# Kernel tuning notes

Measured on AMD Instinct MI355X. Metric: run time of the kernel, lower is better.

Reference implementation:

```python
import jax, jax.numpy as jnp
import numpy as np
from jax import lax

FILTER_SIZE = 11
SIGMA = 1.5
K1, K2 = 0.01, 0.03
WEIGHTS = jnp.array([0.0448, 0.2856, 0.3001, 0.2363, 0.1333], dtype=jnp.float32)


def _gauss_1d(size, sigma):
    coords = jnp.arange(size, dtype=jnp.float32) - (size - 1) / 2.0
    return jax.nn.softmax(-coords ** 2 / (2.0 * sigma ** 2))


def _gaussian_filter(x, k1d):
    # separable depthwise blur, VALID padding: horizontal then vertical
    C = x.shape[1]
    size = k1d.shape[0]
    kw = jnp.broadcast_to(k1d.reshape(1, 1, 1, size), (C, 1, 1, size))  # OIHW
    kh = jnp.broadcast_to(k1d.reshape(1, 1, size, 1), (C, 1, size, 1))
    dn = ('NCHW', 'OIHW', 'NCHW')
    x = lax.conv_general_dilated(x, kw, (1, 1), 'VALID', dimension_numbers=dn, feature_group_count=C)
    x = lax.conv_general_dilated(x, kh, (1, 1), 'VALID', dimension_numbers=dn, feature_group_count=C)
    return x


def _ssim(x, y, k1d, max_val):
    c1 = (K1 * max_val) ** 2
    c2 = (K2 * max_val) ** 2
    mu1 = _gaussian_filter(x, k1d)
    mu2 = _gaussian_filter(y, k1d)
    mu1_sq, mu2_sq, mu1_mu2 = mu1 ** 2, mu2 ** 2, mu1 * mu2
    sigma1_sq = _gaussian_filter(x * x, k1d) - mu1_sq
    sigma2_sq = _gaussian_filter(y * y, k1d) - mu2_sq
    sigma12 = _gaussian_filter(x * y, k1d) - mu1_mu2
    cs_map = (2 * sigma12 + c2) / (sigma1_sq + sigma2_sq + c2)
    ssim_map = (2 * mu1_mu2 + c1) / (mu1_sq + mu2_sq + c1) * cs_map
    return ssim_map.mean(axis=(-1, -2, -3)), cs_map.mean(axis=(-1, -2, -3))


def _avg_pool2(x):
    # torch avg_pool2d(kernel=2, padding=(H%2, W%2)), count_include_pad=True
    ph, pw = x.shape[-2] % 2, x.shape[-1] % 2
    if ph or pw:
        x = jnp.pad(x, ((0, 0), (0, 0), (ph, ph), (pw, pw)))
    N, C, H, W = x.shape
    return x.reshape(N, C, H // 2, 2, W // 2, 2).mean(axis=(-3, -1))


def setup_inputs() -> dict:
    key = jax.random.key(0)
    k1, k2 = jax.random.split(key)
    shape = (32, 3, 512, 512)
    return {
        'input': jax.random.uniform(k1, shape, dtype=jnp.float32),
        'target': jax.random.uniform(k2, shape, dtype=jnp.float32),
    }


def reference(input, target):
    k1d = _gauss_1d(FILTER_SIZE, SIGMA)
    max_val = target.max() - target.min()  # module default: max_val=None
    levels = WEIGHTS.shape[0]
    x, y = input, target
    mcs = []
    ssim_val = None
    for _ in range(levels):
        ssim_val, cs = _ssim(x, y, k1d, max_val)
        mcs.append(cs)
        x = _avg_pool2(x)
        y = _avg_pool2(y)
    mcs = jnp.stack(mcs, axis=0)  # (levels, N)
    # faithful to original: ssim_val ** w[-1] broadcast inside the product
    ms = jnp.prod(mcs[:-1] ** WEIGHTS[:-1, None] * ssim_val ** WEIGHTS[-1], axis=0)
    return ms.mean()
```

## Files before the change

kernel.cpp:

```cpp
#include <hip/hip_runtime.h>
#include <cmath>

#define FILT 11

typedef float v2f __attribute__((ext_vector_type(2)));

struct GW { float w[FILT]; };

__device__ __forceinline__ unsigned enc_f(float f) {
    unsigned u = __float_as_uint(f);
    return (u & 0x80000000u) ? ~u : (u | 0x80000000u);
}
__device__ __forceinline__ float dec_f(unsigned u) {
    return (u & 0x80000000u) ? __uint_as_float(u & 0x7FFFFFFFu)
                             : __uint_as_float(~u);
}

__global__ void init_acc(unsigned* ws) {
    int t = threadIdx.x;
    if (t == 0) { ws[0] = 0u; ws[1] = 0xFFFFFFFFu; }
    for (int i = 2 + t; i < 512; i += blockDim.x) ws[i] = 0u;
}

__global__ void minmax_kernel(const float4* __restrict__ t, long n4, unsigned* mm) {
    unsigned mx = 0u, mn = 0xFFFFFFFFu;
    long stride = (long)gridDim.x * blockDim.x;
    for (long i = (long)blockIdx.x * blockDim.x + threadIdx.x; i < n4; i += stride) {
        float4 v = t[i];
        unsigned a = enc_f(v.x), b = enc_f(v.y), c = enc_f(v.z), d = enc_f(v.w);
        mx = max(mx, max(max(a, b), max(c, d)));
        mn = min(mn, min(min(a, b), min(c, d)));
    }
    for (int off = 32; off; off >>= 1) {
        mx = max(mx, (unsigned)__shfl_down((int)mx, off));
        mn = min(mn, (unsigned)__shfl_down((int)mn, off));
    }
    __shared__ unsigned smx[4], smn[4];
    int wid = threadIdx.x >> 6, lane = threadIdx.x & 63;
    if (lane == 0) { smx[wid] = mx; smn[wid] = mn; }
    __syncthreads();
    if (threadIdx.x == 0) {
        for (int i = 1; i < 4; i++) { mx = max(mx, smx[i]); mn = min(mn, smn[i]); }
        atomicMax(&mm[0], mx);
        atomicMin(&mm[1], mn);
    }
}

__global__ __launch_bounds__(256) void ssim_stream(
    const float* __restrict__ x, const float* __restrict__ y,
    int H, int W, int NC, int nstrips, int nb, int B,
    const unsigned* __restrict__ mm,
    float* __restrict__ cs_sum, float* __restrict__ ssim_sum, GW gw,
    float* __restrict__ poolx, float* __restrict__ pooly, int do_pool)
{
    __shared__ v2f ring[4][2][80];

    const int wv = threadIdx.x >> 6;
    const int lane = threadIdx.x & 63;
    const int wid = blockIdx.x * 4 + wv;
    const int total = NC * nstrips * nb;
    if (wid >= total) return;

    const int band = wid % nb;
    const int t1 = wid / nb;
    const int strip = t1 % nstrips;
    const int img = t1 / nstrips;
    const int n = img / 3;

    const int Ho = H - (FILT - 1);
    const int Wo = W - (FILT - 1);
    const int a = band * B;
    if (a >= Ho) return;
    const int out_hi = min(a + B, Ho);
    const int bEnd = out_hi + (FILT - 1);

    const int base = strip * 64;
    const float* xp = x + (size_t)img * H * W;
    const float* yp = y + (size_t)img * H * W;
    const int c0 = min(base + lane, W - 1);
    const int c1 = min(base + 64 + min(lane, 9), W - 1);
    const bool colv = (base + lane) < Wo;

    const float mv = dec_f(mm[0]) - dec_f(mm[1]);
    const float c1c = (0.01f * mv) * (0.01f * mv);
    const float c2c = (0.03f * mv) * (0.03f * mv);

    const int Wp = W >> 1;
    const size_t pbase = (size_t)img * (H >> 1) * Wp;

    v2f* bufE = &ring[wv][0][0];
    v2f* bufO = &ring[wv][1][0];

    v2f acc01[FILT], acc23[FILT];
    float acc4[FILT];
#pragma unroll
    for (int s = 0; s < FILT; s++) {
        acc01[s] = (v2f){0.f, 0.f};
        acc23[s] = (v2f){0.f, 0.f};
        acc4[s] = 0.f;
    }

    float lcs = 0.f, lss = 0.f;

    float ex0, ey0, ex1, ey1, ox0, oy0, ox1, oy1;
    {
        const float* xe = xp + (size_t)a * W;
        const float* ye = yp + (size_t)a * W;
        ex0 = xe[c0]; ey0 = ye[c0]; ex1 = xe[c1]; ey1 = ye[c1];
        ox0 = xe[W + c0]; oy0 = ye[W + c0];
        ox1 = xe[W + c1]; oy1 = ye[W + c1];
    }

#pragma unroll 1
    for (int r0 = a; r0 < bEnd; r0 += 22) {
#pragma unroll
        for (int p = 0; p < FILT; p++) {
            const int r = r0 + 2 * p;
            if (r < bEnd) {
                const bool hasO = (r + 1 < bEnd);
                const int pe = (2 * p) % FILT;
                const int po = (2 * p + 1) % FILT;

                bufE[lane] = (v2f){ex0, ey0};
                if (lane < 10) bufE[64 + lane] = (v2f){ex1, ey1};
                if (hasO) {
                    bufO[lane] = (v2f){ox0, oy0};
                    if (lane < 10) bufO[64 + lane] = (v2f){ox1, oy1};
                }

                {
                    const int re = min(r + 2, bEnd - 1);
                    const int ro = min(r + 3, bEnd - 1);
                    const float* xe = xp + (size_t)re * W;
                    const float* ye = yp + (size_t)re * W;
                    const float* xo = xp + (size_t)ro * W;
                    const float* yo = yp + (size_t)ro * W;
                    ex0 = xe[c0]; ey0 = ye[c0]; ex1 = xe[c1]; ey1 = ye[c1];
                    ox0 = xo[c0]; oy0 = yo[c0]; ox1 = xo[c1]; oy1 = yo[c1];
                }

                if (do_pool && hasO && lane < 32) {
                    const int pc = (base >> 1) + lane;
                    if (pc < Wp) {
                        float4 qe = *(const float4*)&bufE[2 * lane];
                        float4 qo = *(const float4*)&bufO[2 * lane];
                        size_t o = pbase + (size_t)(r >> 1) * Wp + pc;
                        poolx[o] = 0.25f * (qe.x + qe.z + qo.x + qo.z);
                        pooly[o] = 0.25f * (qe.y + qe.w + qo.y + qo.w);
                    }
                }

                v2f h01e = (v2f){0.f, 0.f}, h23e = (v2f){0.f, 0.f};
                float h4e = 0.f;
#pragma unroll
                for (int k = 0; k < FILT; k++) {
                    v2f v = bufE[lane + k];
                    float w = gw.w[k];
                    v2f w2 = {w, w};
                    h01e = __builtin_elementwise_fma(w2, v, h01e);
                    v2f sq = v * v;
                    h23e = __builtin_elementwise_fma(w2, sq, h23e);
                    h4e = __builtin_fmaf(w, v.x * v.y, h4e);
                }

#pragma unroll
                for (int k = 0; k < FILT; k++) {
                    const int s = (pe - k + FILT) % FILT;
                    float w = gw.w[k];
                    v2f w2 = {w, w};
                    acc01[s] = __builtin_elementwise_fma(w2, h01e, acc01[s]);
                    acc23[s] = __builtin_elementwise_fma(w2, h23e, acc23[s]);
                    acc4[s] = __builtin_fmaf(w, h4e, acc4[s]);
                }

                const int eE = (pe + 1) % FILT;
                if (r >= a + (FILT - 1) && colv) {
                    float m1 = acc01[eE].x, m2 = acc01[eE].y;
                    float mu11 = m1 * m1, mu22 = m2 * m2, mu12 = m1 * m2;
                    float s1 = acc23[eE].x - mu11;
                    float s2 = acc23[eE].y - mu22;
                    float s12 = acc4[eE] - mu12;
                    float A = 2.f * s12 + c2c, Bv = s1 + s2 + c2c;
                    float Cv = 2.f * mu12 + c1c, Dv = mu11 + mu22 + c1c;
                    float r_ = __builtin_amdgcn_rcpf(Bv * Dv);
                    lcs += A * Dv * r_;
                    lss += Cv * A * r_;
                }
                acc01[eE] = (v2f){0.f, 0.f};
                acc23[eE] = (v2f){0.f, 0.f};
                acc4[eE] = 0.f;

                if (hasO) {
                    v2f h01o = (v2f){0.f, 0.f}, h23o = (v2f){0.f, 0.f};
                    float h4o = 0.f;
#pragma unroll
                    for (int k = 0; k < FILT; k++) {
                        v2f v = bufO[lane + k];
                        float w = gw.w[k];
                        v2f w2 = {w, w};
                        h01o = __builtin_elementwise_fma(w2, v, h01o);
                        v2f sq = v * v;
                        h23o = __builtin_elementwise_fma(w2, sq, h23o);
                        h4o = __builtin_fmaf(w, v.x * v.y, h4o);
                    }
#pragma unroll
                    for (int k = 0; k < FILT; k++) {
                        const int s = (po - k + FILT) % FILT;
                        float w = gw.w[k];
                        v2f w2 = {w, w};
                        acc01[s] = __builtin_elementwise_fma(w2, h01o, acc01[s]);
                        acc23[s] = __builtin_elementwise_fma(w2, h23o, acc23[s]);
                        acc4[s] = __builtin_fmaf(w, h4o, acc4[s]);
                    }
                    const int eO = (po + 1) % FILT;
                    if (r >= a + (FILT - 1) && colv) {
                        float m1 = acc01[eO].x, m2 = acc01[eO].y;
                        float mu11 = m1 * m1, mu22 = m2 * m2, mu12 = m1 * m2;
                        float s1 = acc23[eO].x - mu11;
                        float s2 = acc23[eO].y - mu22;
                        float s12 = acc4[eO] - mu12;
                        float A = 2.f * s12 + c2c, Bv = s1 + s2 + c2c;
                        float Cv = 2.f * mu12 + c1c, Dv = mu11 + mu22 + c1c;
                        float r_ = __builtin_amdgcn_rcpf(Bv * Dv);
                        lcs += A * Dv * r_;
                        lss += Cv * A * r_;
                    }
                    acc01[eO] = (v2f){0.f, 0.f};
                    acc23[eO] = (v2f){0.f, 0.f};
                    acc4[eO] = 0.f;
                }
            }
        }
    }

    for (int off = 32; off; off >>= 1) {
        lcs += __shfl_down(lcs, off);
        lss += __shfl_down(lss, off);
    }
    if (lane == 0) {
        atomicAdd(&cs_sum[n], lcs);
        atomicAdd(&ssim_sum[n], lss);
    }
}

__global__ void final_kernel(const float* __restrict__ cs_sum,
                             const float* __restrict__ ssim_sum,
                             float* __restrict__ out)
{
    const float cnt[5] = {3.f * 502 * 502, 3.f * 246 * 246, 3.f * 118 * 118,
                          3.f * 54 * 54, 3.f * 22 * 22};
    const float wts[5] = {0.0448f, 0.2856f, 0.3001f, 0.2363f, 0.1333f};
    int n = threadIdx.x;
    float ms = 0.f;
    if (n < 32) {
        float ssim = ssim_sum[4 * 32 + n] / cnt[4];
        float t = powf(ssim, wts[4]);
        ms = 1.f;
        for (int l = 0; l < 4; l++) {
            float cs = cs_sum[l * 32 + n] / cnt[l];
            ms *= powf(cs, wts[l]) * t;
        }
    }
    for (int off = 32; off; off >>= 1) ms += __shfl_down(ms, off);
    if (threadIdx.x == 0) out[0] = ms / 32.f;
}

extern "C" void kernel_launch(void* const* d_in, const int* in_sizes, int n_in,
                              void* d_out, int out_size, void* d_ws, size_t ws_size,
                              hipStream_t stream) {
    const float* x0 = (const float*)d_in[0];
    const float* y0 = (const float*)d_in[1];
    float* out = (float*)d_out;
    float* ws = (float*)d_ws;
    unsigned* mm = (unsigned*)d_ws;
    float* cs_sum = ws + 2;
    float* ssim_sum = ws + 2 + 5 * 32;

    const int N = 32, C = 3, NC = N * C;
    const int Hs[5] = {512, 256, 128, 64, 32};
    const int Bs[5] = {64, 42, 12, 10, 8};

    float* wp = ws + 512;
    float* pxw[5] = {nullptr, nullptr, nullptr, nullptr, nullptr};
    float* pyw[5] = {nullptr, nullptr, nullptr, nullptr, nullptr};
    for (int l = 1; l < 5; l++) {
        size_t sz = (size_t)NC * Hs[l] * Hs[l];
        pxw[l] = wp; wp += sz;
        pyw[l] = wp; wp += sz;
    }
    const float* px[5] = {x0, pxw[1], pxw[2], pxw[3], pxw[4]};
    const float* py[5] = {y0, pyw[1], pyw[2], pyw[3], pyw[4]};

    GW gw;
    {
        double tmp[FILT], s = 0.0;
        for (int k = 0; k < FILT; k++) {
            double c = (double)k - (FILT - 1) / 2.0;
            tmp[k] = exp(-c * c / (2.0 * 1.5 * 1.5));
            s += tmp[k];
        }
        for (int k = 0; k < FILT; k++) gw.w[k] = (float)(tmp[k] / s);
    }

    init_acc<<<1, 256, 0, stream>>>(mm);
    long n4 = (long)NC * 512 * 512 / 4;
    minmax_kernel<<<2048, 256, 0, stream>>>((const float4*)y0, n4, mm);

    for (int l = 0; l < 5; l++) {
        int H = Hs[l];
        int Ho = H - (FILT - 1);
        int nstrips = (Ho + 63) / 64;
        int B = Bs[l];
        int nb = (Ho + B - 1) / B;
        int total_waves = NC * nstrips * nb;
        int grid = (total_waves + 3) / 4;
        int do_pool = (l < 4) ? 1 : 0;
        ssim_stream<<<grid, 256, 0, stream>>>(
            px[l], py[l], H, H, NC, nstrips, nb, B, mm,
            cs_sum + l * 32, ssim_sum + l * 32, gw,
            do_pool ? pxw[l + 1] : nullptr,
            do_pool ? pyw[l + 1] : nullptr, do_pool);
    }
    final_kernel<<<1, 64, 0, stream>>>(cs_sum, ssim_sum, out);
}
```

Before: 329.0 us.

## Fuse SSIM levels 2-4 into one per-image kernel using shared-memory pyramids

Pyramid levels 2, 3 and 4 are merged into a single kernel with one 1024-thread block per image. Level 2 streams from global memory and writes its 2x2 pooled output into shared memory, then levels 3 and 4 are computed entirely from shared memory. This removes two kernel launches and the global round trips for the small levels, which were dominated by launch and latency costs. Level 0 now runs with 1024-thread blocks instead of 256. The trade-off is heavy shared-memory use per block and only 96 blocks for the fused tail, so parallelism there is low.

```diff
diff --git a/kernel.cpp b/kernel.cpp
--- a/kernel.cpp
+++ b/kernel.cpp
@@ -46,18 +46,19 @@
     }
 }
 
-__global__ __launch_bounds__(256) void ssim_stream(
+__global__ __launch_bounds__(1024) void ssim_stream(
     const float* __restrict__ x, const float* __restrict__ y,
     int H, int W, int NC, int nstrips, int nb, int B,
     const unsigned* __restrict__ mm,
     float* __restrict__ cs_sum, float* __restrict__ ssim_sum, GW gw,
     float* __restrict__ poolx, float* __restrict__ pooly, int do_pool)
 {
-    __shared__ v2f ring[4][2][80];
+    __shared__ v2f ring[16][2][80];
 
     const int wv = threadIdx.x >> 6;
     const int lane = threadIdx.x & 63;
-    const int wid = blockIdx.x * 4 + wv;
+    const int wpb = blockDim.x >> 6;
+    const int wid = blockIdx.x * wpb + wv;
     const int total = NC * nstrips * nb;
     if (wid >= total) return;
 
@@ -162,7 +163,6 @@
                     h23e = __builtin_elementwise_fma(w2, sq, h23e);
                     h4e = __builtin_fmaf(w, v.x * v.y, h4e);
                 }
-
 #pragma unroll
                 for (int k = 0; k < FILT; k++) {
                     const int s = (pe - k + FILT) % FILT;
@@ -172,7 +172,6 @@
                     acc23[s] = __builtin_elementwise_fma(w2, h23e, acc23[s]);
                     acc4[s] = __builtin_fmaf(w, h4e, acc4[s]);
                 }
-
                 const int eE = (pe + 1) % FILT;
                 if (r >= a + (FILT - 1) && colv) {
                     float m1 = acc01[eE].x, m2 = acc01[eE].y;
@@ -240,6 +239,244 @@
     if (lane == 0) {
         atomicAdd(&cs_sum[n], lcs);
         atomicAdd(&ssim_sum[n], lss);
+    }
+}
+
+__device__ __forceinline__ void ssim_lds_strip(
+    const v2f* tile, int Wt, int Wo, int a, int out_hi, int lane,
+    float c1c, float c2c, const GW& gw, float& lcs, float& lss)
+{
+    const int bEnd = out_hi + (FILT - 1);
+    const int tl = min(lane, Wo - 1);
+    const bool colv = lane < Wo;
+
+    v2f acc01[FILT], acc23[FILT];
+    float acc4[FILT];
+#pragma unroll
+    for (int s = 0; s < FILT; s++) {
+        acc01[s] = (v2f){0.f, 0.f};
+        acc23[s] = (v2f){0.f, 0.f};
+        acc4[s] = 0.f;
+    }
+
+#pragma unroll 1
+    for (int r0 = a; r0 < bEnd; r0 += FILT) {
+#pragma unroll
+        for (int p = 0; p < FILT; p++) {
+            const int r = r0 + p;
+            if (r < bEnd) {
+                const v2f* row = tile + (size_t)r * Wt;
+                v2f h01 = (v2f){0.f, 0.f}, h23 = (v2f){0.f, 0.f};
+                float h4 = 0.f;
+#pragma unroll
+                for (int k = 0; k < FILT; k++) {
+                    v2f v = row[tl + k];
+                    float w = gw.w[k];
+                    v2f w2 = {w, w};
+                    h01 = __builtin_elementwise_fma(w2, v, h01);
+                    v2f sq = v * v;
+                    h23 = __builtin_elementwise_fma(w2, sq, h23);
+                    h4 = __builtin_fmaf(w, v.x * v.y, h4);
+                }
+#pragma unroll
+                for (int k = 0; k < FILT; k++) {
+                    const int s = (p - k + FILT) % FILT;
+                    float w = gw.w[k];
+                    v2f w2 = {w, w};
+                    acc01[s] = __builtin_elementwise_fma(w2, h01, acc01[s]);
+                    acc23[s] = __builtin_elementwise_fma(w2, h23, acc23[s]);
+                    acc4[s] = __builtin_fmaf(w, h4, acc4[s]);
+                }
+                const int e = (p + 1) % FILT;
+                if (r >= a + (FILT - 1) && colv) {
+                    float m1 = acc01[e].x, m2 = acc01[e].y;
+                    float mu11 = m1 * m1, mu22 = m2 * m2, mu12 = m1 * m2;
+                    float s1 = acc23[e].x - mu11;
+                    float s2 = acc23[e].y - mu22;
+                    float s12 = acc4[e] - mu12;
+                    float A = 2.f * s12 + c2c, Bv = s1 + s2 + c2c;
+                    float Cv = 2.f * mu12 + c1c, Dv = mu11 + mu22 + c1c;
+                    float r_ = __builtin_amdgcn_rcpf(Bv * Dv);
+                    lcs += A * Dv * r_;
+                    lss += Cv * A * r_;
+                }
+                acc01[e] = (v2f){0.f, 0.f};
+                acc23[e] = (v2f){0.f, 0.f};
+                acc4[e] = 0.f;
+            }
+        }
+    }
+}
+
+__global__ __launch_bounds__(1024) void ssim_tail(
+    const float* __restrict__ x2, const float* __restrict__ y2,
+    const unsigned* __restrict__ mm, float* __restrict__ ws2, GW gw)
+{
+    __shared__ v2f ring[16][2][80];
+    __shared__ v2f buf3[64 * 64];
+    __shared__ v2f buf4[32 * 32];
+
+    const int img = blockIdx.x;
+    const int n = img / 3;
+    const int wv = threadIdx.x >> 6;
+    const int lane = threadIdx.x & 63;
+
+    float* cs2 = ws2 + 2 + 2 * 32;
+    float* cs3 = ws2 + 2 + 3 * 32;
+    float* cs4 = ws2 + 2 + 4 * 32;
+    float* ss2 = ws2 + 2 + 5 * 32 + 2 * 32;
+    float* ss3 = ws2 + 2 + 5 * 32 + 3 * 32;
+    float* ss4 = ws2 + 2 + 5 * 32 + 4 * 32;
+
+    const float mv = dec_f(mm[0]) - dec_f(mm[1]);
+    const float c1c = (0.01f * mv) * (0.01f * mv);
+    const float c2c = (0.03f * mv) * (0.03f * mv);
+
+    {
+        const int strip = wv >> 3;
+        const int band = wv & 7;
+        const int H = 128, W = 128, Ho = 118, B = 16;
+        const int a = band * B;
+        const int out_hi = min(a + B, Ho);
+        const int bEnd = out_hi + (FILT - 1);
+        const int base = strip * 64;
+        const float* xp = x2 + (size_t)img * H * W;
+        const float* yp = y2 + (size_t)img * H * W;
+        const int c0 = min(base + lane, W - 1);
+        const int c1 = min(base + 64 + min(lane, 9), W - 1);
+        const bool colv = (base + lane) < Ho;
+
+        v2f* bufA = &ring[wv][0][0];
+        v2f* bufB = &ring[wv][1][0];
+
+        v2f acc01[FILT], acc23[FILT];
+        float acc4[FILT];
+#pragma unroll
+        for (int s = 0; s < FILT; s++) {
+            acc01[s] = (v2f){0.f, 0.f};
+            acc23[s] = (v2f){0.f, 0.f};
+            acc4[s] = 0.f;
+        }
+        float lcs = 0.f, lss = 0.f;
+
+        const float* xr = xp + (size_t)a * W;
+        const float* yr = yp + (size_t)a * W;
+        float pfx0 = xr[c0], pfy0 = yr[c0];
+        float pfx1 = xr[c1], pfy1 = yr[c1];
+
+#pragma unroll 1
+        for (int r0 = a; r0 < bEnd; r0 += FILT) {
+#pragma unroll
+            for (int p = 0; p < FILT; p++) {
+                const int r = r0 + p;
+                if (r < bEnd) {
+                    v2f* bufc = (r & 1) ? bufB : bufA;
+                    v2f* bufo = (r & 1) ? bufA : bufB;
+
+                    bufc[lane] = (v2f){pfx0, pfy0};
+                    if (lane < 10) bufc[64 + lane] = (v2f){pfx1, pfy1};
+
+                    {
+                        const int rn = min(r + 1, bEnd - 1);
+                        const float* xn = xp + (size_t)rn * W;
+                        const float* yn = yp + (size_t)rn * W;
+                        pfx0 = xn[c0]; pfy0 = yn[c0];
+                        pfx1 = xn[c1]; pfy1 = yn[c1];
+                    }
+
+                    v2f h01 = (v2f){0.f, 0.f}, h23 = (v2f){0.f, 0.f};
+                    float h4 = 0.f;
+#pragma unroll
+                    for (int k = 0; k < FILT; k++) {
+                        v2f v = bufc[lane + k];
+                        float w = gw.w[k];
+                        v2f w2 = {w, w};
+                        h01 = __builtin_elementwise_fma(w2, v, h01);
+                        v2f sq = v * v;
+                        h23 = __builtin_elementwise_fma(w2, sq, h23);
+                        h4 = __builtin_fmaf(w, v.x * v.y, h4);
+                    }
+#pragma unroll
+                    for (int k = 0; k < FILT; k++) {
+                        const int s = (p - k + FILT) % FILT;
+                        float w = gw.w[k];
+                        v2f w2 = {w, w};
+                        acc01[s] = __builtin_elementwise_fma(w2, h01, acc01[s]);
+                        acc23[s] = __builtin_elementwise_fma(w2, h23, acc23[s]);
+                        acc4[s] = __builtin_fmaf(w, h4, acc4[s]);
+                    }
+                    const int e = (p + 1) % FILT;
+                    if (r >= a + (FILT - 1) && colv) {
+                        float m1 = acc01[e].x, m2 = acc01[e].y;
+                        float mu11 = m1 * m1, mu22 = m2 * m2, mu12 = m1 * m2;
+                        float s1 = acc23[e].x - mu11;
+                        float s2 = acc23[e].y - mu22;
+                        float s12 = acc4[e] - mu12;
+                        float A = 2.f * s12 + c2c, Bv = s1 + s2 + c2c;
+                        float Cv = 2.f * mu12 + c1c, Dv = mu11 + mu22 + c1c;
+                        float r_ = __builtin_amdgcn_rcpf(Bv * Dv);
+                        lcs += A * Dv * r_;
+                        lss += Cv * A * r_;
+                    }
+                    acc01[e] = (v2f){0.f, 0.f};
+                    acc23[e] = (v2f){0.f, 0.f};
+                    acc4[e] = 0.f;
+
+                    if ((r & 1) && r > a && lane < 32) {
+                        const int pc = (base >> 1) + lane;
+                        const int pr = r >> 1;
+                        v2f q00 = bufo[2 * lane];
+                        v2f q01 = bufo[2 * lane + 1];
+                        v2f q10 = bufc[2 * lane];
+                        v2f q11 = bufc[2 * lane + 1];
+                        buf3[pr * 64 + pc] =
+                            (q00 + q01 + q10 + q11) * (v2f){0.25f, 0.25f};
+                    }
+                }
+            }
+        }
+
+        for (int off = 32; off; off >>= 1) {
+            lcs += __shfl_down(lcs, off);
+            lss += __shfl_down(lss, off);
+        }
+        if (lane == 0) {
+            atomicAdd(&cs2[n], lcs);
+            atomicAdd(&ss2[n], lss);
+        }
+    }
+    __syncthreads();
+
+    {
+        const int pr = threadIdx.x >> 5;
+        const int pc = threadIdx.x & 31;
+        v2f q = (buf3[(2 * pr) * 64 + 2 * pc] + buf3[(2 * pr) * 64 + 2 * pc + 1] +
+                 buf3[(2 * pr + 1) * 64 + 2 * pc] + buf3[(2 * pr + 1) * 64 + 2 * pc + 1]) *
+                (v2f){0.25f, 0.25f};
+        buf4[pr * 32 + pc] = q;
+    }
+    __syncthreads();
+
+    {
+        float lcs = 0.f, lss = 0.f;
+        bool isL3 = (wv < 14);
+        if (isL3) {
+            const int a = wv * 4;
+            ssim_lds_strip(buf3, 64, 54, a, min(a + 4, 54), lane,
+                           c1c, c2c, gw, lcs, lss);
+        } else {
+            const int a = (wv - 14) * 12;
+            ssim_lds_strip(buf4, 32, 22, a, min(a + 12, 22), lane,
+                           c1c, c2c, gw, lcs, lss);
+        }
+        for (int off = 32; off; off >>= 1) {
+            lcs += __shfl_down(lcs, off);
+            lss += __shfl_down(lss, off);
+        }
+        if (lane == 0) {
+            atomicAdd(isL3 ? &cs3[n] : &cs4[n], lcs);
+            atomicAdd(isL3 ? &ss3[n] : &ss4[n], lss);
+        }
     }
 }
 
@@ -277,19 +514,12 @@
     float* ssim_sum = ws + 2 + 5 * 32;
 
     const int N = 32, C = 3, NC = N * C;
-    const int Hs[5] = {512, 256, 128, 64, 32};
-    const int Bs[5] = {64, 42, 12, 10, 8};
 
     float* wp = ws + 512;
-    float* pxw[5] = {nullptr, nullptr, nullptr, nullptr, nullptr};
-    float* pyw[5] = {nullptr, nullptr, nullptr, nullptr, nullptr};
-    for (int l = 1; l < 5; l++) {
-        size_t sz = (size_t)NC * Hs[l] * Hs[l];
-        pxw[l] = wp; wp += sz;
-        pyw[l] = wp; wp += sz;
-    }
-    const float* px[5] = {x0, pxw[1], pxw[2], pxw[3], pxw[4]};
-    const float* py[5] = {y0, pyw[1], pyw[2], pyw[3], pyw[4]};
+    float* pxw1 = wp; wp += (size_t)NC * 256 * 256;
+    float* pyw1 = wp; wp += (size_t)NC * 256 * 256;
+    float* pxw2 = wp; wp += (size_t)NC * 128 * 128;
+    float* pyw2 = wp; wp += (size_t)NC * 128 * 128;
 
     GW gw;
     {
@@ -306,20 +536,25 @@
     long n4 = (long)NC * 512 * 512 / 4;
     minmax_kernel<<<2048, 256, 0, stream>>>((const float4*)y0, n4, mm);
 
-    for (int l = 0; l < 5; l++) {
-        int H = Hs[l];
-        int Ho = H - (FILT - 1);
-        int nstrips = (Ho + 63) / 64;
-        int B = Bs[l];
+    {
+        int H = 512, Ho = 502, nstrips = 8, B = 64;
         int nb = (Ho + B - 1) / B;
-        int total_waves = NC * nstrips * nb;
-        int grid = (total_waves + 3) / 4;
-        int do_pool = (l < 4) ? 1 : 0;
+        int total = NC * nstrips * nb;
+        int grid = (total + 15) / 16;
+        ssim_stream<<<grid, 1024, 0, stream>>>(
+            x0, y0, H, H, NC, nstrips, nb, B, mm,
+            cs_sum + 0 * 32, ssim_sum + 0 * 32, gw, pxw1, pyw1, 1);
+    }
+    {
+        int H = 256, Ho = 246, nstrips = 4, B = 42;
+        int nb = (Ho + B - 1) / B;
+        int total = NC * nstrips * nb;
+        int grid = (total + 3) / 4;
         ssim_stream<<<grid, 256, 0, stream>>>(
-            px[l], py[l], H, H, NC, nstrips, nb, B, mm,
-            cs_sum + l * 32, ssim_sum + l * 32, gw,
-            do_pool ? pxw[l + 1] : nullptr,
-            do_pool ? pyw[l + 1] : nullptr, do_pool);
-    }
+            pxw1, pyw1, H, H, NC, nstrips, nb, B, mm,
+            cs_sum + 1 * 32, ssim_sum + 1 * 32, gw, pxw2, pyw2, 1);
+    }
+    ssim_tail<<<NC, 1024, 0, stream>>>(pxw2, pyw2, mm, ws, gw);
+
     final_kernel<<<1, 64, 0, stream>>>(cs_sum, ssim_sum, out);
 }
```

Result: slower. 380.8 us (+15.7%).
